# Kernel optimization log

Hardware: AMD Instinct MI355X
Metric: run time of the kernel (lower is better)

Reference implementation:

```python
import jax, jax.numpy as jnp
import numpy as np

MU = 5
ETA = 1.0
ITERATIONS = 3


def _sobel(x):
    # torch F.conv2d is cross-correlation; replicate exactly
    k = jnp.array([[-1., 0., 1.], [-2., 0., 2.], [-1., 0., 1.]], dtype=x.dtype)
    kernel = jnp.stack([k, k.T])[:, None]  # [2,1,3,3] OIHW
    return jax.lax.conv_general_dilated(
        x, kernel, window_strides=(1, 1), padding=[(1, 1), (1, 1)],
        dimension_numbers=('NCHW', 'OIHW', 'NCHW'))


def _cnorm(v):
    # 2-norm over channel dim, keepdim
    return jnp.sqrt(jnp.sum(v * v, axis=1, keepdims=True))


def setup_inputs() -> dict:
    key = jax.random.key(0)
    inputs = jax.random.uniform(key, (8, 1, 1024, 1024), dtype=jnp.float32)
    return {"inputs": inputs}


def reference(inputs):
    B, _, H, W = inputs.shape
    pad = ((0, 0), (0, 0), (MU, MU), (MU, MU))

    sobel = _sobel(inputs)                       # [B,2,H,W]
    sobel_mag = _cnorm(sobel)                    # [B,1,H,W]
    sobel_mag = sobel_mag / jnp.max(sobel_mag)
    sobel_mag_p = jnp.pad(sobel_mag, pad)

    # tang = flip(sobel, ch) * [-1, 1] -> perpendicular (tangent) field
    tang = jnp.stack([-sobel[:, 1], sobel[:, 0]], axis=1)
    tmag = _cnorm(tang)
    tang = tang / jnp.where(tmag == 0, jnp.ones_like(tmag), tmag)

    for _it in range(ITERATIONS):
        for ori in ('V', 'H'):
            tang_p = jnp.pad(tang, pad)
            tang_X = tang
            acc = jnp.zeros_like(tang)
            for i in range(2 * MU + 1):
                if ori == 'V':
                    tang_Y = tang_p[:, :, i:i + H, MU:MU + W]
                    sob_Y = sobel_mag_p[:, :, i:i + H, MU:MU + W]
                else:
                    tang_Y = tang_p[:, :, MU:MU + H, i:i + W]
                    sob_Y = sobel_mag_p[:, :, MU:MU + H, i:i + W]
                w = (jnp.tanh(ETA * (sob_Y - sobel_mag)) + 1.0) \
                    * jnp.sum(tang_X * tang_Y, axis=1, keepdims=True) * 0.5
                acc = acc + tang_Y * w
            tang = acc
        tmag = _cnorm(tang)
        tang = tang / jnp.where(tmag == 0, jnp.ones_like(tmag), tmag)
    return tang
```

## Files before the change

kernel.cpp:

```cpp
#include <hip/hip_runtime.h>

#define MU 5
static constexpr int Hh = 1024, Ww = 1024, Bb = 8;
static constexpr int NPIX = Bb * Hh * Ww;
static constexpr int TPB = 256;
static constexpr int SPY = 4;
static constexpr int SOBEL_BLOCKS = NPIX / SPY / TPB;

static constexpr int TX = 64, TY = 32;
static constexpr int VW = TX + 2 * MU;
static constexpr int ER = TY + 2 * MU;
static constexpr int EPITCH = 76;
static constexpr int FBLK = (Ww / TX) * (Hh / TY) * Bb;

__device__ __forceinline__ float rcp_fast(float x) { return __builtin_amdgcn_rcpf(x); }
__device__ __forceinline__ float rsq_fast(float x) { return __builtin_amdgcn_rsqf(x); }

__global__ __launch_bounds__(TPB) void sobel_kernel(
        const float* __restrict__ in, float2* __restrict__ tang,
        float* __restrict__ mag, float* __restrict__ partials) {
    int id = blockIdx.x * TPB + threadIdx.x;
    int x = id & (Ww - 1);
    int yg = (id >> 10) & (Hh / SPY - 1);
    int b = id >> 18;
    int y0 = yg * SPY;
    const float* p = in + ((size_t)b << 20);

    float a[SPY + 2][3];
    bool cl = (x > 0), cr = (x < Ww - 1);
    if (yg >= 1 && yg <= Hh / SPY - 2) {
        #pragma unroll
        for (int r = 0; r < SPY + 2; ++r) {
            const float* row = p + (y0 - 1 + r) * Ww + x;
            a[r][0] = cl ? row[-1] : 0.0f;
            a[r][1] = row[0];
            a[r][2] = cr ? row[1] : 0.0f;
        }
    } else {
        #pragma unroll
        for (int r = 0; r < SPY + 2; ++r) {
            int yy = y0 - 1 + r;
            bool okr = (yy >= 0) && (yy < Hh);
            const float* row = p + (okr ? yy : 0) * Ww + x;
            a[r][0] = (okr && cl) ? row[-1] : 0.0f;
            a[r][1] = okr ? row[0] : 0.0f;
            a[r][2] = (okr && cr) ? row[1] : 0.0f;
        }
    }

    float s[SPY + 2];
    #pragma unroll
    for (int r = 0; r < SPY + 2; ++r) s[r] = a[r][2] - a[r][0];

    float vmax = 0.0f;
    #pragma unroll
    for (int k = 0; k < SPY; ++k) {
        float gx = s[k] + 2.0f * s[k + 1] + s[k + 2];
        float u1 = a[k + 2][0] - a[k][0];
        float u2 = a[k + 2][1] - a[k][1];
        float u3 = a[k + 2][2] - a[k][2];
        float gy = u1 + 2.0f * u2 + u3;
        float g2 = gx * gx + gy * gy;
        float irs = rsq_fast(g2);
        float m   = (g2 > 0.0f) ? g2 * irs : 0.0f;
        float inv = (g2 > 0.0f) ? irs : 1.0f;
        int j = (b << 20) + (y0 + k) * Ww + x;
        mag[j] = m;
        tang[j] = make_float2(-gy * inv, gx * inv);
        vmax = fmaxf(vmax, m);
    }

    #pragma unroll
    for (int off = 32; off; off >>= 1) vmax = fmaxf(vmax, __shfl_xor(vmax, off));
    __shared__ float smax[4];
    int lane = threadIdx.x & 63, wid = threadIdx.x >> 6;
    if (lane == 0) smax[wid] = vmax;
    __syncthreads();
    if (threadIdx.x == 0)
        partials[blockIdx.x] = fmaxf(fmaxf(smax[0], smax[1]), fmaxf(smax[2], smax[3]));
}

__global__ void max_reduce_kernel(const float* __restrict__ partials,
                                  float* __restrict__ scale_out) {
    float v = 0.0f;
    for (int i = threadIdx.x; i < SOBEL_BLOCKS; i += 1024)
        v = fmaxf(v, partials[i]);
    #pragma unroll
    for (int off = 32; off; off >>= 1) v = fmaxf(v, __shfl_xor(v, off));
    __shared__ float smax[16];
    int lane = threadIdx.x & 63, wid = threadIdx.x >> 6;
    if (lane == 0) smax[wid] = v;
    __syncthreads();
    if (threadIdx.x == 0) {
        float m = smax[0];
        #pragma unroll
        for (int i = 1; i < 16; ++i) m = fmaxf(m, smax[i]);
        *scale_out = 1.0f / m;
    }
}

__global__ void prep_kernel(float4* __restrict__ mag4,
                            const float* __restrict__ scalep) {
    int id = blockIdx.x * blockDim.x + threadIdx.x;
    float k = 2.0f * (*scalep);
    float4 m = mag4[id];
    m.x = __expf(k * m.x);
    m.y = __expf(k * m.y);
    m.z = __expf(k * m.z);
    m.w = __expf(k * m.w);
    mag4[id] = m;
}

template <bool FINAL>
__global__ __launch_bounds__(TPB) void etf_fused(const float2* __restrict__ src,
                                                 float2* __restrict__ dstI,
                                                 float* __restrict__ dstP,
                                                 const float* __restrict__ E) {
    __shared__ float2 vT[TY][VW];
    __shared__ float  eT[ER][EPITCH];

    int bid = (int)blockIdx.x;
    int swz = (bid & 7) * (FBLK / 8) + (bid >> 3);
    int img = swz >> 9;
    int cid = swz & 511;
    int tx = cid >> 5, ty = cid & 31;
    int x0 = tx * TX, y0 = ty * TY;
    int base = img << 20;
    int t = threadIdx.x;

    for (int i = t; i < ER * VW; i += TPB) {
        int r = i / VW, c = i % VW;
        int gy = y0 - MU + r, gx = x0 - MU + c;
        bool ok = (gy >= 0) && (gy < Hh) && (gx >= 0) && (gx < Ww);
        eT[r][c] = ok ? E[base + gy * Ww + gx] : 1.0f;
    }
    __syncthreads();

    for (int task = t; task < VW * (TY / 8); task += TPB) {
        int c = task % VW;
        int g = task / VW;
        int gx = x0 - MU + c;
        int yb = y0 + g * 8;
        if (gx < 0 || gx >= Ww) {
            #pragma unroll
            for (int k = 0; k < 8; ++k) vT[g * 8 + k][c] = make_float2(0.0f, 0.0f);
            continue;
        }
        float2 tt[18]; float ee[18];
        if (yb - MU >= 0 && yb + 13 <= Hh) {
            #pragma unroll
            for (int rr = 0; rr < 18; ++rr) {
                tt[rr] = src[base + (yb - MU + rr) * Ww + gx];
                ee[rr] = eT[8 * g + rr][c];
            }
        } else {
            #pragma unroll
            for (int rr = 0; rr < 18; ++rr) {
                int row = yb - MU + rr;
                bool ok = (row >= 0) && (row < Hh);
                tt[rr] = ok ? src[base + row * Ww + gx] : make_float2(0.0f, 0.0f);
                ee[rr] = ok ? eT[8 * g + rr][c] : 1.0f;
            }
        }
        #pragma unroll
        for (int k = 0; k < 8; ++k) {
            float2 tX = tt[k + MU];
            float  eX = ee[k + MU];
            float ax = 0.0f, ay = 0.0f;
            #pragma unroll
            for (int i = 0; i <= 2 * MU; ++i) {
                float2 tY = tt[k + i];
                float  eY = ee[k + i];
                float d = tX.x * tY.x + tX.y * tY.y;
                float w = eY * rcp_fast(eX + eY) * d;
                ax += tY.x * w;
                ay += tY.y * w;
            }
            vT[g * 8 + k][c] = make_float2(ax, ay);
        }
    }
    __syncthreads();

    int r = t >> 3;
    int cb = (t & 7) * 8;
    float2 wv[18]; float we[18];
    #pragma unroll
    for (int q = 0; q < 18; ++q) {
        wv[q] = vT[r][cb + q];
        we[q] = eT[r + MU][cb + q];
    }
    float ox[8], oy[8];
    #pragma unroll
    for (int j = 0; j < 8; ++j) {
        float2 tX = wv[j + MU];
        float  eX = we[j + MU];
        float ax = 0.0f, ay = 0.0f;
        #pragma unroll
        for (int i = 0; i <= 2 * MU; ++i) {
            float2 tY = wv[j + i];
            float  eY = we[j + i];
            float d = tX.x * tY.x + tX.y * tY.y;
            float w = eY * rcp_fast(eX + eY) * d;
            ax += tY.x * w;
            ay += tY.y * w;
        }
        float n2 = ax * ax + ay * ay;
        float inv = (n2 > 0.0f) ? rsq_fast(n2) : 1.0f;
        ox[j] = ax * inv;
        oy[j] = ay * inv;
    }

    if (FINAL) {
        size_t p0 = ((size_t)(img * 2 + 0) << 20) + (size_t)(y0 + r) * Ww + x0 + cb;
        size_t p1 = ((size_t)(img * 2 + 1) << 20) + (size_t)(y0 + r) * Ww + x0 + cb;
        *(float4*)&dstP[p0]     = make_float4(ox[0], ox[1], ox[2], ox[3]);
        *(float4*)&dstP[p0 + 4] = make_float4(ox[4], ox[5], ox[6], ox[7]);
        *(float4*)&dstP[p1]     = make_float4(oy[0], oy[1], oy[2], oy[3]);
        *(float4*)&dstP[p1 + 4] = make_float4(oy[4], oy[5], oy[6], oy[7]);
    } else {
        __syncthreads();
        #pragma unroll
        for (int j = 0; j < 8; ++j) vT[r][cb + j] = make_float2(ox[j], oy[j]);
        __syncthreads();
        for (int i = t; i < TY * TX; i += TPB) {
            int rr = i >> 6, cc = i & 63;
            dstI[base + (y0 + rr) * Ww + x0 + cc] = vT[rr][cc];
        }
    }
}

extern "C" void kernel_launch(void* const* d_in, const int* in_sizes, int n_in,
                              void* d_out, int out_size, void* d_ws, size_t ws_size,
                              hipStream_t stream) {
    const float* in = (const float*)d_in[0];
    float* out = (float*)d_out;
    char* ws = (char*)d_ws;

    float* magE = (float*)ws;
    float2* tA = (float2*)(ws + (size_t)NPIX * sizeof(float));
    float* partials = (float*)(ws + (size_t)NPIX * sizeof(float)
                                  + (size_t)NPIX * sizeof(float2));
    float* scalep = partials + SOBEL_BLOCKS;
    float2* tOut = (float2*)out;

    sobel_kernel<<<SOBEL_BLOCKS, TPB, 0, stream>>>(in, tA, magE, partials);
    max_reduce_kernel<<<1, 1024, 0, stream>>>(partials, scalep);
    prep_kernel<<<NPIX / 4 / TPB, TPB, 0, stream>>>((float4*)magE, scalep);

    etf_fused<false><<<FBLK, TPB, 0, stream>>>(tA, tOut, nullptr, magE);
    etf_fused<false><<<FBLK, TPB, 0, stream>>>(tOut, tA, nullptr, magE);
    etf_fused<true ><<<FBLK, TPB, 0, stream>>>(tA, nullptr, out, magE);
}
```

Measured before the change: 259.8 us.

## Vectorize sobel loads and stores, split shared tile into SoA, store directly

The sobel kernel now has each thread handle four horizontally adjacent pixels with float4 loads and stores, replacing four vertical pixels read with scalar loads. The ETF kernel splits the intermediate float2 shared tile into separate x/y float arrays with an odd pitch of 75 to reduce LDS bank conflicts. It also loads the E tile row-per-wave to avoid div/mod indexing, and writes intermediate results straight to global as float4 without the extra shared-memory staging and two barriers. The risks are less coalesced vertical reuse in sobel and direct per-thread strided global writes.

```diff
diff --git a/kernel.cpp b/kernel.cpp
--- a/kernel.cpp
+++ b/kernel.cpp
@@ -4,13 +4,12 @@
 static constexpr int Hh = 1024, Ww = 1024, Bb = 8;
 static constexpr int NPIX = Bb * Hh * Ww;
 static constexpr int TPB = 256;
-static constexpr int SPY = 4;
-static constexpr int SOBEL_BLOCKS = NPIX / SPY / TPB;
+static constexpr int SOBEL_BLOCKS = NPIX / 4 / TPB;
 
 static constexpr int TX = 64, TY = 32;
 static constexpr int VW = TX + 2 * MU;
 static constexpr int ER = TY + 2 * MU;
-static constexpr int EPITCH = 76;
+static constexpr int EP = 75;
 static constexpr int FBLK = (Ww / TX) * (Hh / TY) * Bb;
 
 __device__ __forceinline__ float rcp_fast(float x) { return __builtin_amdgcn_rcpf(x); }
@@ -20,55 +19,52 @@
         const float* __restrict__ in, float2* __restrict__ tang,
         float* __restrict__ mag, float* __restrict__ partials) {
     int id = blockIdx.x * TPB + threadIdx.x;
-    int x = id & (Ww - 1);
-    int yg = (id >> 10) & (Hh / SPY - 1);
-    int b = id >> 18;
-    int y0 = yg * SPY;
+    int xq = id & (Ww / 4 - 1);
+    int x0 = xq * 4;
+    int y  = (id >> 8) & (Hh - 1);
+    int b  = id >> 18;
     const float* p = in + ((size_t)b << 20);
 
-    float a[SPY + 2][3];
-    bool cl = (x > 0), cr = (x < Ww - 1);
-    if (yg >= 1 && yg <= Hh / SPY - 2) {
-        #pragma unroll
-        for (int r = 0; r < SPY + 2; ++r) {
-            const float* row = p + (y0 - 1 + r) * Ww + x;
-            a[r][0] = cl ? row[-1] : 0.0f;
-            a[r][1] = row[0];
-            a[r][2] = cr ? row[1] : 0.0f;
-        }
-    } else {
-        #pragma unroll
-        for (int r = 0; r < SPY + 2; ++r) {
-            int yy = y0 - 1 + r;
-            bool okr = (yy >= 0) && (yy < Hh);
-            const float* row = p + (okr ? yy : 0) * Ww + x;
-            a[r][0] = (okr && cl) ? row[-1] : 0.0f;
-            a[r][1] = okr ? row[0] : 0.0f;
-            a[r][2] = (okr && cr) ? row[1] : 0.0f;
-        }
-    }
-
-    float s[SPY + 2];
-    #pragma unroll
-    for (int r = 0; r < SPY + 2; ++r) s[r] = a[r][2] - a[r][0];
-
+    float c[3][6];
+    #pragma unroll
+    for (int r = 0; r < 3; ++r) {
+        int yy = y - 1 + r;
+        bool okr = (yy >= 0) && (yy < Hh);
+        const float* row = p + (okr ? yy : 0) * Ww;
+        float4 v = okr ? *(const float4*)(row + x0) : make_float4(0.f, 0.f, 0.f, 0.f);
+        c[r][1] = v.x; c[r][2] = v.y; c[r][3] = v.z; c[r][4] = v.w;
+        c[r][0] = (okr && x0 > 0)      ? row[x0 - 1] : 0.0f;
+        c[r][5] = (okr && x0 + 4 < Ww) ? row[x0 + 4] : 0.0f;
+    }
+
+    float S[6], D[6];
+    #pragma unroll
+    for (int cc = 0; cc < 6; ++cc) {
+        S[cc] = c[0][cc] + 2.0f * c[1][cc] + c[2][cc];
+        D[cc] = c[2][cc] - c[0][cc];
+    }
+
+    float2 tg[4];
+    float  mg[4];
     float vmax = 0.0f;
     #pragma unroll
-    for (int k = 0; k < SPY; ++k) {
-        float gx = s[k] + 2.0f * s[k + 1] + s[k + 2];
-        float u1 = a[k + 2][0] - a[k][0];
-        float u2 = a[k + 2][1] - a[k][1];
-        float u3 = a[k + 2][2] - a[k][2];
-        float gy = u1 + 2.0f * u2 + u3;
+    for (int k = 0; k < 4; ++k) {
+        float gx = S[k + 2] - S[k];
+        float gy = D[k] + 2.0f * D[k + 1] + D[k + 2];
         float g2 = gx * gx + gy * gy;
         float irs = rsq_fast(g2);
         float m   = (g2 > 0.0f) ? g2 * irs : 0.0f;
         float inv = (g2 > 0.0f) ? irs : 1.0f;
-        int j = (b << 20) + (y0 + k) * Ww + x;
-        mag[j] = m;
-        tang[j] = make_float2(-gy * inv, gx * inv);
+        mg[k] = m;
+        tg[k] = make_float2(-gy * inv, gx * inv);
         vmax = fmaxf(vmax, m);
     }
+
+    int idx = (b << 20) + y * Ww + x0;
+    *(float4*)&mag[idx] = make_float4(mg[0], mg[1], mg[2], mg[3]);
+    float4* tp = (float4*)&tang[idx];
+    tp[0] = make_float4(tg[0].x, tg[0].y, tg[1].x, tg[1].y);
+    tp[1] = make_float4(tg[2].x, tg[2].y, tg[3].x, tg[3].y);
 
     #pragma unroll
     for (int off = 32; off; off >>= 1) vmax = fmaxf(vmax, __shfl_xor(vmax, off));
@@ -116,8 +112,9 @@
                                                  float2* __restrict__ dstI,
                                                  float* __restrict__ dstP,
                                                  const float* __restrict__ E) {
-    __shared__ float2 vT[TY][VW];
-    __shared__ float  eT[ER][EPITCH];
+    __shared__ float eT[ER][EP];
+    __shared__ float vx[TY][EP];
+    __shared__ float vy[TY][EP];
 
     int bid = (int)blockIdx.x;
     int swz = (bid & 7) * (FBLK / 8) + (bid >> 3);
@@ -127,23 +124,38 @@
     int x0 = tx * TX, y0 = ty * TY;
     int base = img << 20;
     int t = threadIdx.x;
-
-    for (int i = t; i < ER * VW; i += TPB) {
-        int r = i / VW, c = i % VW;
-        int gy = y0 - MU + r, gx = x0 - MU + c;
-        bool ok = (gy >= 0) && (gy < Hh) && (gx >= 0) && (gx < Ww);
-        eT[r][c] = ok ? E[base + gy * Ww + gx] : 1.0f;
-    }
-    __syncthreads();
-
-    for (int task = t; task < VW * (TY / 8); task += TPB) {
-        int c = task % VW;
-        int g = task / VW;
+    int lane = t & 63, wave = t >> 6;
+
+    for (int r = wave; r < ER; r += 4) {
+        int gy = y0 - MU + r;
+        bool okr = (gy >= 0) && (gy < Hh);
+        const float* erow = E + base + gy * Ww + (x0 - MU);
+        {
+            int cc = lane;
+            int gx = x0 - MU + cc;
+            bool ok = okr && (gx >= 0) && (gx < Ww);
+            eT[r][cc] = ok ? erow[cc] : 1.0f;
+        }
+        if (lane < VW - 64) {
+            int cc = 64 + lane;
+            int gx = x0 - MU + cc;
+            bool ok = okr && (gx < Ww);
+            eT[r][cc] = ok ? erow[cc] : 1.0f;
+        }
+    }
+    __syncthreads();
+
+    #pragma unroll
+    for (int round = 0; round < 2; ++round) {
+        int T = t + round * TPB;
+        if (T >= VW * 4) break;
+        int g = T / VW;
+        int c = T - g * VW;
         int gx = x0 - MU + c;
         int yb = y0 + g * 8;
         if (gx < 0 || gx >= Ww) {
             #pragma unroll
-            for (int k = 0; k < 8; ++k) vT[g * 8 + k][c] = make_float2(0.0f, 0.0f);
+            for (int k = 0; k < 8; ++k) { vx[g * 8 + k][c] = 0.0f; vy[g * 8 + k][c] = 0.0f; }
             continue;
         }
         float2 tt[18]; float ee[18];
@@ -151,7 +163,7 @@
             #pragma unroll
             for (int rr = 0; rr < 18; ++rr) {
                 tt[rr] = src[base + (yb - MU + rr) * Ww + gx];
-                ee[rr] = eT[8 * g + rr][c];
+                ee[rr] = eT[g * 8 + rr][c];
             }
         } else {
             #pragma unroll
@@ -159,7 +171,7 @@
                 int row = yb - MU + rr;
                 bool ok = (row >= 0) && (row < Hh);
                 tt[rr] = ok ? src[base + row * Ww + gx] : make_float2(0.0f, 0.0f);
-                ee[rr] = ok ? eT[8 * g + rr][c] : 1.0f;
+                ee[rr] = ok ? eT[g * 8 + rr][c] : 1.0f;
             }
         }
         #pragma unroll
@@ -176,33 +188,35 @@
                 ax += tY.x * w;
                 ay += tY.y * w;
             }
-            vT[g * 8 + k][c] = make_float2(ax, ay);
+            vx[g * 8 + k][c] = ax;
+            vy[g * 8 + k][c] = ay;
         }
     }
     __syncthreads();
 
     int r = t >> 3;
     int cb = (t & 7) * 8;
-    float2 wv[18]; float we[18];
+    float wxv[18], wyv[18], we[18];
     #pragma unroll
     for (int q = 0; q < 18; ++q) {
-        wv[q] = vT[r][cb + q];
-        we[q] = eT[r + MU][cb + q];
+        wxv[q] = vx[r][cb + q];
+        wyv[q] = vy[r][cb + q];
+        we[q]  = eT[r + MU][cb + q];
     }
     float ox[8], oy[8];
     #pragma unroll
     for (int j = 0; j < 8; ++j) {
-        float2 tX = wv[j + MU];
-        float  eX = we[j + MU];
+        float txc = wxv[j + MU], tyc = wyv[j + MU];
+        float eX = we[j + MU];
         float ax = 0.0f, ay = 0.0f;
         #pragma unroll
         for (int i = 0; i <= 2 * MU; ++i) {
-            float2 tY = wv[j + i];
-            float  eY = we[j + i];
-            float d = tX.x * tY.x + tX.y * tY.y;
+            float vxt = wxv[j + i], vyt = wyv[j + i];
+            float eY = we[j + i];
+            float d = txc * vxt + tyc * vyt;
             float w = eY * rcp_fast(eX + eY) * d;
-            ax += tY.x * w;
-            ay += tY.y * w;
+            ax += vxt * w;
+            ay += vyt * w;
         }
         float n2 = ax * ax + ay * ay;
         float inv = (n2 > 0.0f) ? rsq_fast(n2) : 1.0f;
@@ -218,14 +232,11 @@
         *(float4*)&dstP[p1]     = make_float4(oy[0], oy[1], oy[2], oy[3]);
         *(float4*)&dstP[p1 + 4] = make_float4(oy[4], oy[5], oy[6], oy[7]);
     } else {
-        __syncthreads();
-        #pragma unroll
-        for (int j = 0; j < 8; ++j) vT[r][cb + j] = make_float2(ox[j], oy[j]);
-        __syncthreads();
-        for (int i = t; i < TY * TX; i += TPB) {
-            int rr = i >> 6, cc = i & 63;
-            dstI[base + (y0 + rr) * Ww + x0 + cc] = vT[rr][cc];
-        }
+        float4* dp = (float4*)&dstI[base + (y0 + r) * Ww + x0 + cb];
+        dp[0] = make_float4(ox[0], oy[0], ox[1], oy[1]);
+        dp[1] = make_float4(ox[2], oy[2], ox[3], oy[3]);
+        dp[2] = make_float4(ox[4], oy[4], ox[5], oy[5]);
+        dp[3] = make_float4(ox[6], oy[6], ox[7], oy[7]);
     }
 }
 
```

Result: slower. 292.3 us (+12.5%).
